# Performance work log

Measured on AMD Instinct MI355X. Metric: run time of the kernel, lower is better.

Reference implementation:

```python
import jax, jax.numpy as jnp
import numpy as np

K = 3

def setup_inputs() -> dict:
    key = jax.random.key(0)
    k1, k2, k3, k4 = jax.random.split(key, 4)
    B, N, F_in, T, F_out = 8, 2048, 16, 12, 32
    x = jax.random.normal(k1, (B, N, F_in, T), dtype=jnp.float32)
    spatial_attention = jax.random.uniform(k2, (B, N, N), dtype=jnp.float32)
    node_embeddings = jax.random.normal(k3, (N, 16), dtype=jnp.float32)
    theta = jax.random.normal(k4, (K, F_in, F_out), dtype=jnp.float32) * 0.1
    return {"x": x, "spatial_attention": spatial_attention,
            "node_embeddings": node_embeddings, "theta": theta}

def _cheb_polys(node_embeddings, N, K):
    # supports = softmax(relu(E E^T), axis=1)
    supports = jax.nn.softmax(jax.nn.relu(node_embeddings @ node_embeddings.T), axis=1)
    polys = [jnp.eye(N, dtype=supports.dtype), supports]
    for _ in range(2, K):
        polys.append(2.0 * supports @ polys[-1] - polys[-2])
    return jnp.stack(polys[:K], axis=0)  # (K, N, N)

def reference(x, spatial_attention, node_embeddings, theta):
    B, N, F_in, T = x.shape
    polys = _cheb_polys(node_embeddings, N, K)             # (K,N,N)
    # T_k_with_at = polys[k] * attention (broadcast over batch);
    # rhs = T_k_with_at^T @ graph_signal for every timestep:
    # (K,N,N)*(B,N,N) contracted with (B,N,F,T) over source node n -> (K,B,M,F,T)
    rhs = jnp.einsum('knm,bnm,bnft->kbmft', polys, spatial_attention, x)
    # accumulate rhs @ theta_k over k -> (B,M,F_out,T)
    out = jnp.einsum('kbmft,kfo->bmot', rhs, theta)
    return jax.nn.relu(out)
```

## Files before the change

kernel.cpp:

```cpp
#include <hip/hip_runtime.h>

#define NN    2048
#define BATCH 8
#define FIN   16
#define TT    12
#define FOUT  32
#define FT    (FIN*TT)
#define OT    (FOUT*TT)

typedef unsigned short ushort_t;
typedef __attribute__((ext_vector_type(8))) short   short8;
typedef __attribute__((ext_vector_type(4))) float   f32x4;
typedef __attribute__((ext_vector_type(4))) unsigned short us4;
typedef __attribute__((ext_vector_type(8))) unsigned short us8;

__device__ __forceinline__ float b2f(unsigned short u) {
    union { unsigned int i; float f; } v; v.i = ((unsigned int)u) << 16; return v.f;
}
__device__ __forceinline__ unsigned short f2b(float f) {
    union { float f; unsigned int i; } v; v.f = f;
    unsigned int x = v.i;
    x += 0x7fffu + ((x >> 16) & 1u);
    return (unsigned short)(x >> 16);
}

#define LGKM0()   asm volatile("s_waitcnt lgkmcnt(0)" ::: "memory")
#define BARRIER() __builtin_amdgcn_s_barrier()

__global__ __launch_bounds__(256)
void k_supports(const float* __restrict__ E, ushort_t* __restrict__ Sb) {
    const int n = blockIdx.x;
    __shared__ float row[NN];
    __shared__ float red[256];
    const int tid = threadIdx.x;

    const f32x4 en0 = *(const f32x4*)&E[n * 16 + 0];
    const f32x4 en1 = *(const f32x4*)&E[n * 16 + 4];
    const f32x4 en2 = *(const f32x4*)&E[n * 16 + 8];
    const f32x4 en3 = *(const f32x4*)&E[n * 16 + 12];

    float lmax = 0.0f;
    for (int m = tid; m < NN; m += 256) {
        const f32x4* Em = (const f32x4*)&E[(size_t)m * 16];
        const f32x4 e0 = Em[0], e1 = Em[1], e2 = Em[2], e3 = Em[3];
        float d = 0.0f;
        #pragma unroll
        for (int j = 0; j < 4; ++j) d += en0[j] * e0[j];
        #pragma unroll
        for (int j = 0; j < 4; ++j) d += en1[j] * e1[j];
        #pragma unroll
        for (int j = 0; j < 4; ++j) d += en2[j] * e2[j];
        #pragma unroll
        for (int j = 0; j < 4; ++j) d += en3[j] * e3[j];
        d = fmaxf(d, 0.0f);
        row[m] = d;
        lmax = fmaxf(lmax, d);
    }
    red[tid] = lmax; __syncthreads();
    for (int s = 128; s > 0; s >>= 1) {
        if (tid < s) red[tid] = fmaxf(red[tid], red[tid + s]);
        __syncthreads();
    }
    const float mx = red[0];
    __syncthreads();

    float lsum = 0.0f;
    for (int m = tid; m < NN; m += 256) {
        float e = __expf(row[m] - mx);
        row[m] = e;
        lsum += e;
    }
    red[tid] = lsum; __syncthreads();
    for (int s = 128; s > 0; s >>= 1) {
        if (tid < s) red[tid] += red[tid + s];
        __syncthreads();
    }
    const float inv = 1.0f / red[0];
    for (int m = tid; m < NN; m += 256) Sb[(size_t)n * NN + m] = f2b(row[m] * inv);
}

__global__ __launch_bounds__(256)
void k_pack_st(const ushort_t* __restrict__ Sb, ushort_t* __restrict__ SbT) {
    const int r0 = blockIdx.x * 64, c0 = blockIdx.y * 64;
    __shared__ ushort_t Lt[64][65];
    const int tid = threadIdx.x;
    #pragma unroll
    for (int p = 0; p < 2; ++p) {
        const int i = (tid >> 3) + p * 32;
        const int j8 = (tid & 7) * 8;
        us8 v = *(const us8*)&Sb[(size_t)(r0 + i) * NN + c0 + j8];
        #pragma unroll
        for (int e = 0; e < 8; ++e) Lt[i][j8 + e] = v[e];
    }
    __syncthreads();
    #pragma unroll
    for (int p = 0; p < 2; ++p) {
        const int jj = (tid >> 3) + p * 32;
        const int i8 = (tid & 7) * 8;
        us8 v;
        #pragma unroll
        for (int e = 0; e < 8; ++e) v[e] = Lt[i8 + e][jj];
        *(us8*)&SbT[(size_t)(c0 + jj) * NN + r0 + i8] = v;
    }
}

__global__ __launch_bounds__(256)
void k_pack_x(const float* __restrict__ x, ushort_t* __restrict__ xbT) {
    const int nc = blockIdx.x * 64;
    const int b  = blockIdx.y;
    __shared__ ushort_t Lt[FT][65];
    const int tid = threadIdx.x;
    const float* __restrict__ xb = x + (size_t)b * NN * FT;
    #pragma unroll
    for (int p = 0; p < 12; ++p) {
        const int id = tid + 256 * p;
        const int nn = id / 48;
        const int f4 = (id % 48) * 4;
        const float4 v = *(const float4*)&xb[(size_t)(nc + nn) * FT + f4];
        Lt[f4 + 0][nn] = f2b(v.x);
        Lt[f4 + 1][nn] = f2b(v.y);
        Lt[f4 + 2][nn] = f2b(v.z);
        Lt[f4 + 3][nn] = f2b(v.w);
    }
    __syncthreads();
    #pragma unroll
    for (int p = 0; p < 6; ++p) {
        const int id = tid + 256 * p;
        const int ft = id >> 3;
        const int n8 = (id & 7) * 8;
        us8 v;
        #pragma unroll
        for (int e = 0; e < 8; ++e) v[e] = Lt[ft][n8 + e];
        *(us8*)&xbT[((size_t)b * FT + ft) * NN + nc + n8] = v;
    }
}

__global__ __launch_bounds__(256, 4)
void k_t2(const ushort_t* __restrict__ Sb, const ushort_t* __restrict__ SbT,
          ushort_t* __restrict__ T2b) {
    const int m0 = blockIdx.x * 64;
    const int n0 = blockIdx.y * 64;
    __shared__ __align__(16) ushort_t As[2][64 * 64];
    __shared__ __align__(16) ushort_t Bs[2][64 * 64];
    const int tid = threadIdx.x;
    const int lane = tid & 63, w = tid >> 6;
    const int l15 = lane & 15, q = lane >> 4, l7 = lane & 7;
    const int n0w = (w & 1) * 32, m0w = (w >> 1) * 32;
    const int sr = tid >> 3;
    const int sc = tid & 7;

    f32x4 acc[2][2];
    #pragma unroll
    for (int i = 0; i < 2; ++i)
        #pragma unroll
        for (int j = 0; j < 2; ++j) acc[i][j] = {0.f, 0.f, 0.f, 0.f};

    us8 avA[2], bvA[2], avB[2], bvB[2];

#define T2_LOAD(l0, av, bv)                                              \
    { _Pragma("unroll") for (int p = 0; p < 2; ++p) {                    \
        const int row_ = sr + 32 * p;                                    \
        av[p] = *(const us8*)&Sb[(size_t)(n0 + row_) * NN + (l0) + sc * 8];  \
        bv[p] = *(const us8*)&SbT[(size_t)(m0 + row_) * NN + (l0) + sc * 8]; \
      } }

#define T2_STORE(bufi, av, bv)                                           \
    { _Pragma("unroll") for (int p = 0; p < 2; ++p) {                    \
        const int row_ = sr + 32 * p;                                    \
        const int cs_ = (sc ^ (row_ & 7)) * 8;                           \
        *(us8*)&As[bufi][row_ * 64 + cs_] = av[p];                       \
        *(us8*)&Bs[bufi][row_ * 64 + cs_] = bv[p];                       \
      } }

#define T2_MFMA(bufi)                                                    \
    { _Pragma("unroll") for (int s = 0; s < 2; ++s) {                    \
        short8 a_[2], b_[2];                                             \
        const int u_ = ((s * 4 + q) ^ l7) * 8;                           \
        _Pragma("unroll") for (int i = 0; i < 2; ++i)                    \
            a_[i] = *(const short8*)&As[bufi][(n0w + i * 16 + l15) * 64 + u_]; \
        _Pragma("unroll") for (int j = 0; j < 2; ++j)                    \
            b_[j] = *(const short8*)&Bs[bufi][(m0w + j * 16 + l15) * 64 + u_]; \
        _Pragma("unroll") for (int i = 0; i < 2; ++i)                    \
            _Pragma("unroll") for (int j = 0; j < 2; ++j)                \
                acc[i][j] = __builtin_amdgcn_mfma_f32_16x16x32_bf16(a_[i], b_[j], acc[i][j], 0, 0, 0); \
      } }

    T2_LOAD(0, avA, bvA);
    T2_LOAD(64, avB, bvB);
    T2_STORE(0, avA, bvA);

    for (int it = 0; it < 32; it += 2) {
        LGKM0(); BARRIER();
        if (it < 30) T2_LOAD((it + 2) * 64, avA, bvA);
        T2_MFMA(0);
        T2_STORE(1, avB, bvB);
        LGKM0(); BARRIER();
        if (it < 29) T2_LOAD((it + 3) * 64, avB, bvB);
        T2_MFMA(1);
        if (it < 30) T2_STORE(0, avA, bvA);
    }
#undef T2_LOAD
#undef T2_STORE
#undef T2_MFMA

    #pragma unroll
    for (int i = 0; i < 2; ++i)
        #pragma unroll
        for (int j = 0; j < 2; ++j)
            #pragma unroll
            for (int r = 0; r < 4; ++r) {
                const int ng = n0 + n0w + i * 16 + q * 4 + r;
                const int mg = m0 + m0w + j * 16 + l15;
                const float v = 2.0f * acc[i][j][r] - (ng == mg ? 1.0f : 0.0f);
                T2b[(size_t)ng * NN + mg] = f2b(v);
            }
}

__global__ __launch_bounds__(256, 1)
void k_rhs(const ushort_t* __restrict__ Sb, const ushort_t* __restrict__ T2b,
           const float* __restrict__ att, const ushort_t* __restrict__ xbT,
           float* __restrict__ rhs) {
    const int m0 = blockIdx.x * 64;
    const int b  = blockIdx.y;
    __shared__ __align__(16) ushort_t As[128 * 64];
    __shared__ __align__(16) ushort_t Xs[2][FT * 64];
    const int tid = threadIdx.x;
    const int lane = tid & 63, w = tid >> 6;
    const int l15 = lane & 15, q = lane >> 4, l7 = lane & 7, l3 = lane >> 3;
    const int k1 = w & 1, ft0 = (w >> 1) * 96;
    const float* __restrict__ attb = att + (size_t)b * NN * NN;

    const int k1s = tid >> 7;
    const int uu  = tid & 127;
    const int m4  = (uu & 15) * 4;
    const int nn8 = (uu >> 4) * 8;
    const ushort_t* __restrict__ Pk = k1s ? T2b : Sb;

    f32x4 acc[4][6];
    #pragma unroll
    for (int i = 0; i < 4; ++i)
        #pragma unroll
        for (int t = 0; t < 6; ++t) acc[i][t] = {0.f, 0.f, 0.f, 0.f};

    us8   xv[6];
    us4   pv[8];
    f32x4 av[8];

#define RHS_LOADX(nc)                                                       \
    { _Pragma("unroll") for (int p = 0; p < 6; ++p) {                       \
        const int row_ = (w * 6 + p) * 8 + l3;                              \
        xv[p] = *(const us8*)&xbT[((size_t)b * FT + row_) * NN + (nc) + l7 * 8]; \
      } }

#define RHS_LOADPA(nc)                                                      \
    { _Pragma("unroll") for (int r = 0; r < 8; ++r) {                       \
        const int nn_ = (nc) + nn8 + r;                                     \
        pv[r] = *(const us4*)&Pk[(size_t)nn_ * NN + m0 + m4];               \
        av[r] = *(const f32x4*)&attb[(size_t)nn_ * NN + m0 + m4];           \
      } }

#define RHS_WRITE_XS(bufi)                                                  \
    { _Pragma("unroll") for (int p = 0; p < 6; ++p) {                       \
        const int row_ = (w * 6 + p) * 8 + l3;                              \
        *(us8*)&Xs[bufi][row_ * 64 + (l7 ^ l3) * 8] = xv[p];                \
      } }

#define RHS_WRITE_AS()                                                      \
    { _Pragma("unroll") for (int c = 0; c < 4; ++c) {                       \
        const int rowm_ = m4 + c;                                           \
        const int g_ = (nn8 >> 3) ^ (rowm_ & 7);                            \
        unsigned int u0_, u1_, u2_, u3_;                                    \
        { const float a_ = b2f(pv[0][c]) * av[0][c];                        \
          const float b_ = b2f(pv[1][c]) * av[1][c];                        \
          asm("v_cvt_pk_bf16_f32 %0, %1, %2" : "=v"(u0_) : "v"(a_), "v"(b_)); } \
        { const float a_ = b2f(pv[2][c]) * av[2][c];                        \
          const float b_ = b2f(pv[3][c]) * av[3][c];                        \
          asm("v_cvt_pk_bf16_f32 %0, %1, %2" : "=v"(u1_) : "v"(a_), "v"(b_)); } \
        { const float a_ = b2f(pv[4][c]) * av[4][c];                        \
          const float b_ = b2f(pv[5][c]) * av[5][c];                        \
          asm("v_cvt_pk_bf16_f32 %0, %1, %2" : "=v"(u2_) : "v"(a_), "v"(b_)); } \
        { const float a_ = b2f(pv[6][c]) * av[6][c];                        \
          const float b_ = b2f(pv[7][c]) * av[7][c];                        \
          asm("v_cvt_pk_bf16_f32 %0, %1, %2" : "=v"(u3_) : "v"(a_), "v"(b_)); } \
        *(uint4*)&As[(k1s * 64 + rowm_) * 64 + g_ * 8] =                    \
            make_uint4(u0_, u1_, u2_, u3_);                                 \
      } }

#define RHS_MFMA(bufi)                                                      \
    { _Pragma("unroll") for (int s = 0; s < 2; ++s) {                       \
        short8 a_[4], bb_[6];                                               \
        _Pragma("unroll") for (int i = 0; i < 4; ++i) {                     \
            const int rw_ = i * 16 + l15;                                   \
            a_[i] = *(const short8*)&As[(k1 * 64 + rw_) * 64 + (((s * 4 + q) ^ l7) * 8)]; \
        }                                                                   \
        _Pragma("unroll") for (int t = 0; t < 6; ++t) {                     \
            const int col_ = ft0 + t * 16 + l15;                            \
            const int u_ = ((s * 4 + q) ^ (col_ & 7)) * 8;                  \
            bb_[t] = *(const short8*)&Xs[bufi][col_ * 64 + u_];             \
        }                                                                   \
        _Pragma("unroll") for (int i = 0; i < 4; ++i)                       \
            _Pragma("unroll") for (int t = 0; t < 6; ++t)                   \
                acc[i][t] = __builtin_amdgcn_mfma_f32_16x16x32_bf16(a_[i], bb_[t], acc[i][t], 0, 0, 0); \
      } }

    RHS_LOADX(0);
    RHS_LOADPA(0);
    RHS_WRITE_XS(0);

    for (int c = 0; c < 32; ++c) {
        LGKM0(); BARRIER();
        RHS_WRITE_AS();
        if (c < 31) {
            RHS_LOADX((c + 1) * 64);
            RHS_LOADPA((c + 1) * 64);
        }
        LGKM0(); BARRIER();
        RHS_MFMA(c & 1);
        if (c < 31) RHS_WRITE_XS((c + 1) & 1);
    }
#undef RHS_LOADX
#undef RHS_LOADPA
#undef RHS_WRITE_XS
#undef RHS_WRITE_AS
#undef RHS_MFMA

    float* __restrict__ op = rhs + ((size_t)(k1 * BATCH + b)) * NN * FT;
    #pragma unroll
    for (int i = 0; i < 4; ++i)
        #pragma unroll
        for (int t = 0; t < 6; ++t)
            #pragma unroll
            for (int r = 0; r < 4; ++r) {
                const int mg = m0 + i * 16 + q * 4 + r;
                const int ftg = ft0 + t * 16 + l15;
                op[(size_t)mg * FT + ftg] = acc[i][t][r];
            }
}

__global__ __launch_bounds__(128)
void k_out(const float* __restrict__ x, const float* __restrict__ att,
           const float* __restrict__ theta, const float* __restrict__ rhs,
           float* __restrict__ out) {
    const int m = blockIdx.x & (NN - 1);
    const int b = blockIdx.x >> 11;
    __shared__ float xr[FT], r1[FT], r2[FT];
    __shared__ float th[3 * FIN * FOUT];
    const int tid = threadIdx.x;

    const float* __restrict__ xb = x + ((size_t)b * NN + m) * FT;
    const float* __restrict__ p1 = rhs + ((size_t)0 * BATCH + b) * NN * FT + (size_t)m * FT;
    const float* __restrict__ p2 = rhs + ((size_t)1 * BATCH + b) * NN * FT + (size_t)m * FT;
    const float a0 = att[((size_t)b * NN + m) * NN + m];

    for (int i = tid; i < FT; i += 128) {
        xr[i] = xb[i] * a0;
        r1[i] = p1[i];
        r2[i] = p2[i];
    }
    for (int i = tid; i < 3 * FIN * FOUT; i += 128) th[i] = theta[i];
    __syncthreads();

    float* __restrict__ ob = out + ((size_t)b * NN + m) * OT;
    for (int idx = tid; idx < OT; idx += 128) {
        const int o = idx / TT, t = idx % TT;
        float acc = 0.0f;
        #pragma unroll
        for (int f = 0; f < FIN; ++f) {
            const int ft = f * TT + t;
            acc += th[f * FOUT + o] * xr[ft];
            acc += th[512 + f * FOUT + o] * r1[ft];
            acc += th[1024 + f * FOUT + o] * r2[ft];
        }
        ob[idx] = fmaxf(acc, 0.0f);
    }
}

extern "C" void kernel_launch(void* const* d_in, const int* in_sizes, int n_in,
                              void* d_out, int out_size, void* d_ws, size_t ws_size,
                              hipStream_t stream) {
    const float* x     = (const float*)d_in[0];
    const float* att   = (const float*)d_in[1];
    const float* E     = (const float*)d_in[2];
    const float* theta = (const float*)d_in[3];
    float* out = (float*)d_out;

    ushort_t* Sb  = (ushort_t*)d_ws;
    ushort_t* SbT = Sb  + (size_t)NN * NN;
    ushort_t* T2b = SbT + (size_t)NN * NN;
    ushort_t* xbT = T2b + (size_t)NN * NN;
    float*    rhs = (float*)(xbT + (size_t)BATCH * FT * NN);

    k_supports<<<NN, 256, 0, stream>>>(E, Sb);
    k_pack_st<<<dim3(32, 32), 256, 0, stream>>>(Sb, SbT);
    k_pack_x<<<dim3(32, BATCH), 256, 0, stream>>>(x, xbT);
    k_t2<<<dim3(32, 32), 256, 0, stream>>>(Sb, SbT, T2b);
    k_rhs<<<dim3(32, BATCH), 256, 0, stream>>>(Sb, T2b, att, xbT, rhs);
    k_out<<<BATCH * NN, 128, 0, stream>>>(x, att, theta, rhs, out);
}
```

Before: 331.6 us.

## Enlarge k_t2 tiles to 128x128 and double-buffer k_rhs across 512 threads

```diff
diff --git a/kernel.cpp b/kernel.cpp
--- a/kernel.cpp
+++ b/kernel.cpp
@@ -135,23 +135,24 @@
     }
 }
 
-__global__ __launch_bounds__(256, 4)
+__global__ __launch_bounds__(512, 2)
 void k_t2(const ushort_t* __restrict__ Sb, const ushort_t* __restrict__ SbT,
           ushort_t* __restrict__ T2b) {
-    const int m0 = blockIdx.x * 64;
-    const int n0 = blockIdx.y * 64;
-    __shared__ __align__(16) ushort_t As[2][64 * 64];
-    __shared__ __align__(16) ushort_t Bs[2][64 * 64];
+    const int m0 = blockIdx.x * 128;
+    const int n0 = blockIdx.y * 128;
+    __shared__ __align__(16) ushort_t As[2][128 * 64];
+    __shared__ __align__(16) ushort_t Bs[2][128 * 64];
     const int tid = threadIdx.x;
     const int lane = tid & 63, w = tid >> 6;
     const int l15 = lane & 15, q = lane >> 4, l7 = lane & 7;
-    const int n0w = (w & 1) * 32, m0w = (w >> 1) * 32;
+    const int nw = (w & 1) * 64;
+    const int mw = (w >> 1) * 32;
     const int sr = tid >> 3;
     const int sc = tid & 7;
 
-    f32x4 acc[2][2];
-    #pragma unroll
-    for (int i = 0; i < 2; ++i)
+    f32x4 acc[4][2];
+    #pragma unroll
+    for (int i = 0; i < 4; ++i)
         #pragma unroll
         for (int j = 0; j < 2; ++j) acc[i][j] = {0.f, 0.f, 0.f, 0.f};
 
@@ -159,14 +160,14 @@
 
 #define T2_LOAD(l0, av, bv)                                              \
     { _Pragma("unroll") for (int p = 0; p < 2; ++p) {                    \
-        const int row_ = sr + 32 * p;                                    \
+        const int row_ = sr + 64 * p;                                    \
         av[p] = *(const us8*)&Sb[(size_t)(n0 + row_) * NN + (l0) + sc * 8];  \
         bv[p] = *(const us8*)&SbT[(size_t)(m0 + row_) * NN + (l0) + sc * 8]; \
       } }
 
 #define T2_STORE(bufi, av, bv)                                           \
     { _Pragma("unroll") for (int p = 0; p < 2; ++p) {                    \
-        const int row_ = sr + 32 * p;                                    \
+        const int row_ = sr + 64 * p;                                    \
         const int cs_ = (sc ^ (row_ & 7)) * 8;                           \
         *(us8*)&As[bufi][row_ * 64 + cs_] = av[p];                       \
         *(us8*)&Bs[bufi][row_ * 64 + cs_] = bv[p];                       \
@@ -174,13 +175,13 @@
 
 #define T2_MFMA(bufi)                                                    \
     { _Pragma("unroll") for (int s = 0; s < 2; ++s) {                    \
-        short8 a_[2], b_[2];                                             \
+        short8 a_[4], b_[2];                                             \
         const int u_ = ((s * 4 + q) ^ l7) * 8;                           \
-        _Pragma("unroll") for (int i = 0; i < 2; ++i)                    \
-            a_[i] = *(const short8*)&As[bufi][(n0w + i * 16 + l15) * 64 + u_]; \
+        _Pragma("unroll") for (int i = 0; i < 4; ++i)                    \
+            a_[i] = *(const short8*)&As[bufi][(nw + i * 16 + l15) * 64 + u_]; \
         _Pragma("unroll") for (int j = 0; j < 2; ++j)                    \
-            b_[j] = *(const short8*)&Bs[bufi][(m0w + j * 16 + l15) * 64 + u_]; \
-        _Pragma("unroll") for (int i = 0; i < 2; ++i)                    \
+            b_[j] = *(const short8*)&Bs[bufi][(mw + j * 16 + l15) * 64 + u_]; \
+        _Pragma("unroll") for (int i = 0; i < 4; ++i)                    \
             _Pragma("unroll") for (int j = 0; j < 2; ++j)                \
                 acc[i][j] = __builtin_amdgcn_mfma_f32_16x16x32_bf16(a_[i], b_[j], acc[i][j], 0, 0, 0); \
       } }
@@ -188,147 +189,134 @@
     T2_LOAD(0, avA, bvA);
     T2_LOAD(64, avB, bvB);
     T2_STORE(0, avA, bvA);
-
-    for (int it = 0; it < 32; it += 2) {
+    T2_LOAD(128, avA, bvA);
+    LGKM0(); BARRIER();
+
+    for (int c = 0; c < 32; c += 2) {
+        T2_MFMA(0);
+        if (c < 31) T2_STORE(1, avB, bvB);
+        if (c < 29) T2_LOAD((c + 3) * 64, avB, bvB);
         LGKM0(); BARRIER();
-        if (it < 30) T2_LOAD((it + 2) * 64, avA, bvA);
-        T2_MFMA(0);
-        T2_STORE(1, avB, bvB);
+        T2_MFMA(1);
+        if (c < 30) T2_STORE(0, avA, bvA);
+        if (c < 28) T2_LOAD((c + 4) * 64, avA, bvA);
         LGKM0(); BARRIER();
-        if (it < 29) T2_LOAD((it + 3) * 64, avB, bvB);
-        T2_MFMA(1);
-        if (it < 30) T2_STORE(0, avA, bvA);
     }
 #undef T2_LOAD
 #undef T2_STORE
 #undef T2_MFMA
 
     #pragma unroll
-    for (int i = 0; i < 2; ++i)
+    for (int i = 0; i < 4; ++i)
         #pragma unroll
         for (int j = 0; j < 2; ++j)
             #pragma unroll
             for (int r = 0; r < 4; ++r) {
-                const int ng = n0 + n0w + i * 16 + q * 4 + r;
-                const int mg = m0 + m0w + j * 16 + l15;
+                const int ng = n0 + nw + i * 16 + q * 4 + r;
+                const int mg = m0 + mw + j * 16 + l15;
                 const float v = 2.0f * acc[i][j][r] - (ng == mg ? 1.0f : 0.0f);
                 T2b[(size_t)ng * NN + mg] = f2b(v);
             }
 }
 
-__global__ __launch_bounds__(256, 1)
+__global__ __launch_bounds__(512, 2)
 void k_rhs(const ushort_t* __restrict__ Sb, const ushort_t* __restrict__ T2b,
            const float* __restrict__ att, const ushort_t* __restrict__ xbT,
            float* __restrict__ rhs) {
     const int m0 = blockIdx.x * 64;
     const int b  = blockIdx.y;
-    __shared__ __align__(16) ushort_t As[128 * 64];
+    __shared__ __align__(16) ushort_t As[2][128 * 64];
     __shared__ __align__(16) ushort_t Xs[2][FT * 64];
     const int tid = threadIdx.x;
     const int lane = tid & 63, w = tid >> 6;
     const int l15 = lane & 15, q = lane >> 4, l7 = lane & 7, l3 = lane >> 3;
-    const int k1 = w & 1, ft0 = (w >> 1) * 96;
+    const int k1 = w & 1, ft0 = (w >> 1) * 48;
     const float* __restrict__ attb = att + (size_t)b * NN * NN;
 
-    const int k1s = tid >> 7;
-    const int uu  = tid & 127;
+    const int k1s = tid >> 8;
+    const int uu  = tid & 255;
     const int m4  = (uu & 15) * 4;
-    const int nn8 = (uu >> 4) * 8;
+    const int nn4 = (uu >> 4) * 4;
     const ushort_t* __restrict__ Pk = k1s ? T2b : Sb;
 
-    f32x4 acc[4][6];
+    f32x4 acc[4][3];
     #pragma unroll
     for (int i = 0; i < 4; ++i)
         #pragma unroll
-        for (int t = 0; t < 6; ++t) acc[i][t] = {0.f, 0.f, 0.f, 0.f};
-
-    us8   xv[6];
-    us4   pv[8];
-    f32x4 av[8];
-
-#define RHS_LOADX(nc)                                                       \
-    { _Pragma("unroll") for (int p = 0; p < 6; ++p) {                       \
-        const int row_ = (w * 6 + p) * 8 + l3;                              \
+        for (int t = 0; t < 3; ++t) acc[i][t] = {0.f, 0.f, 0.f, 0.f};
+
+    us8   xvA[3], xvB[3];
+    us4   pvA[4], pvB[4];
+    f32x4 avA[4], avB[4];
+
+#define RHS_LOAD(nc, xv, pv, av)                                            \
+    { _Pragma("unroll") for (int p = 0; p < 3; ++p) {                       \
+        const int row_ = (w * 3 + p) * 8 + l3;                              \
         xv[p] = *(const us8*)&xbT[((size_t)b * FT + row_) * NN + (nc) + l7 * 8]; \
-      } }
-
-#define RHS_LOADPA(nc)                                                      \
-    { _Pragma("unroll") for (int r = 0; r < 8; ++r) {                       \
-        const int nn_ = (nc) + nn8 + r;                                     \
+      }                                                                     \
+      _Pragma("unroll") for (int r = 0; r < 4; ++r) {                       \
+        const int nn_ = (nc) + nn4 + r;                                     \
         pv[r] = *(const us4*)&Pk[(size_t)nn_ * NN + m0 + m4];               \
         av[r] = *(const f32x4*)&attb[(size_t)nn_ * NN + m0 + m4];           \
       } }
 
-#define RHS_WRITE_XS(bufi)                                                  \
-    { _Pragma("unroll") for (int p = 0; p < 6; ++p) {                       \
-        const int row_ = (w * 6 + p) * 8 + l3;                              \
+#define RHS_WRITE(bufi, xv, pv, av)                                         \
+    { _Pragma("unroll") for (int p = 0; p < 3; ++p) {                       \
+        const int row_ = (w * 3 + p) * 8 + l3;                              \
         *(us8*)&Xs[bufi][row_ * 64 + (l7 ^ l3) * 8] = xv[p];                \
-      } }
-
-#define RHS_WRITE_AS()                                                      \
-    { _Pragma("unroll") for (int c = 0; c < 4; ++c) {                       \
-        const int rowm_ = m4 + c;                                           \
-        const int g_ = (nn8 >> 3) ^ (rowm_ & 7);                            \
-        unsigned int u0_, u1_, u2_, u3_;                                    \
-        { const float a_ = b2f(pv[0][c]) * av[0][c];                        \
-          const float b_ = b2f(pv[1][c]) * av[1][c];                        \
-          asm("v_cvt_pk_bf16_f32 %0, %1, %2" : "=v"(u0_) : "v"(a_), "v"(b_)); } \
-        { const float a_ = b2f(pv[2][c]) * av[2][c];                        \
-          const float b_ = b2f(pv[3][c]) * av[3][c];                        \
-          asm("v_cvt_pk_bf16_f32 %0, %1, %2" : "=v"(u1_) : "v"(a_), "v"(b_)); } \
-        { const float a_ = b2f(pv[4][c]) * av[4][c];                        \
-          const float b_ = b2f(pv[5][c]) * av[5][c];                        \
-          asm("v_cvt_pk_bf16_f32 %0, %1, %2" : "=v"(u2_) : "v"(a_), "v"(b_)); } \
-        { const float a_ = b2f(pv[6][c]) * av[6][c];                        \
-          const float b_ = b2f(pv[7][c]) * av[7][c];                        \
-          asm("v_cvt_pk_bf16_f32 %0, %1, %2" : "=v"(u3_) : "v"(a_), "v"(b_)); } \
-        *(uint4*)&As[(k1s * 64 + rowm_) * 64 + g_ * 8] =                    \
-            make_uint4(u0_, u1_, u2_, u3_);                                 \
+      }                                                                     \
+      _Pragma("unroll") for (int c_ = 0; c_ < 4; ++c_) {                    \
+        const int rowm_ = m4 + c_;                                          \
+        const int g_ = (nn4 >> 3) ^ (rowm_ & 7);                            \
+        unsigned int u01_, u23_;                                            \
+        { const float a_ = b2f(pv[0][c_]) * av[0][c_];                      \
+          const float b_ = b2f(pv[1][c_]) * av[1][c_];                      \
+          asm("v_cvt_pk_bf16_f32 %0, %1, %2" : "=v"(u01_) : "v"(a_), "v"(b_)); } \
+        { const float a_ = b2f(pv[2][c_]) * av[2][c_];                      \
+          const float b_ = b2f(pv[3][c_]) * av[3][c_];                      \
+          asm("v_cvt_pk_bf16_f32 %0, %1, %2" : "=v"(u23_) : "v"(a_), "v"(b_)); } \
+        *(uint2*)&As[bufi][(k1s * 64 + rowm_) * 64 + g_ * 8 + (nn4 & 4)] =  \
+            make_uint2(u01_, u23_);                                         \
       } }
 
 #define RHS_MFMA(bufi)                                                      \
     { _Pragma("unroll") for (int s = 0; s < 2; ++s) {                       \
-        short8 a_[4], bb_[6];                                               \
-        _Pragma("unroll") for (int i = 0; i < 4; ++i) {                     \
-            const int rw_ = i * 16 + l15;                                   \
-            a_[i] = *(const short8*)&As[(k1 * 64 + rw_) * 64 + (((s * 4 + q) ^ l7) * 8)]; \
-        }                                                                   \
-        _Pragma("unroll") for (int t = 0; t < 6; ++t) {                     \
-            const int col_ = ft0 + t * 16 + l15;                            \
-            const int u_ = ((s * 4 + q) ^ (col_ & 7)) * 8;                  \
-            bb_[t] = *(const short8*)&Xs[bufi][col_ * 64 + u_];             \
-        }                                                                   \
+        short8 a_[4], bb_[3];                                               \
+        const int u_ = ((s * 4 + q) ^ l7) * 8;                              \
         _Pragma("unroll") for (int i = 0; i < 4; ++i)                       \
-            _Pragma("unroll") for (int t = 0; t < 6; ++t)                   \
+            a_[i] = *(const short8*)&As[bufi][(k1 * 64 + i * 16 + l15) * 64 + u_]; \
+        _Pragma("unroll") for (int t = 0; t < 3; ++t)                       \
+            bb_[t] = *(const short8*)&Xs[bufi][(ft0 + t * 16 + l15) * 64 + u_]; \
+        _Pragma("unroll") for (int i = 0; i < 4; ++i)                       \
+            _Pragma("unroll") for (int t = 0; t < 3; ++t)                   \
                 acc[i][t] = __builtin_amdgcn_mfma_f32_16x16x32_bf16(a_[i], bb_[t], acc[i][t], 0, 0, 0); \
       } }
 
-    RHS_LOADX(0);
-    RHS_LOADPA(0);
-    RHS_WRITE_XS(0);
-
-    for (int c = 0; c < 32; ++c) {
+    RHS_LOAD(0, xvA, pvA, avA);
+    RHS_LOAD(64, xvB, pvB, avB);
+    RHS_WRITE(0, xvA, pvA, avA);
+    RHS_LOAD(128, xvA, pvA, avA);
+    LGKM0(); BARRIER();
+
+    for (int c = 0; c < 32; c += 2) {
+        RHS_MFMA(0);
+        if (c < 31) RHS_WRITE(1, xvB, pvB, avB);
+        if (c < 29) RHS_LOAD((c + 3) * 64, xvB, pvB, avB);
         LGKM0(); BARRIER();
-        RHS_WRITE_AS();
-        if (c < 31) {
-            RHS_LOADX((c + 1) * 64);
-            RHS_LOADPA((c + 1) * 64);
-        }
+        RHS_MFMA(1);
+        if (c < 30) RHS_WRITE(0, xvA, pvA, avA);
+        if (c < 28) RHS_LOAD((c + 4) * 64, xvA, pvA, avA);
         LGKM0(); BARRIER();
-        RHS_MFMA(c & 1);
-        if (c < 31) RHS_WRITE_XS((c + 1) & 1);
-    }
-#undef RHS_LOADX
-#undef RHS_LOADPA
-#undef RHS_WRITE_XS
-#undef RHS_WRITE_AS
+    }
+#undef RHS_LOAD
+#undef RHS_WRITE
 #undef RHS_MFMA
 
     float* __restrict__ op = rhs + ((size_t)(k1 * BATCH + b)) * NN * FT;
     #pragma unroll
     for (int i = 0; i < 4; ++i)
         #pragma unroll
-        for (int t = 0; t < 6; ++t)
+        for (int t = 0; t < 3; ++t)
             #pragma unroll
             for (int r = 0; r < 4; ++r) {
                 const int mg = m0 + i * 16 + q * 4 + r;
@@ -393,7 +381,7 @@
     k_supports<<<NN, 256, 0, stream>>>(E, Sb);
     k_pack_st<<<dim3(32, 32), 256, 0, stream>>>(Sb, SbT);
     k_pack_x<<<dim3(32, BATCH), 256, 0, stream>>>(x, xbT);
-    k_t2<<<dim3(32, 32), 256, 0, stream>>>(Sb, SbT, T2b);
-    k_rhs<<<dim3(32, BATCH), 256, 0, stream>>>(Sb, T2b, att, xbT, rhs);
+    k_t2<<<dim3(16, 16), 512, 0, stream>>>(Sb, SbT, T2b);
+    k_rhs<<<dim3(32, BATCH), 512, 0, stream>>>(Sb, T2b, att, xbT, rhs);
     k_out<<<BATCH * NN, 128, 0, stream>>>(x, att, theta, rhs, out);
 }
```

New measurement: 320.6 us. 3.3% less time.
